# Kernel tuning notes

Measured on AMD Instinct MI355X. Metric: run time of the kernel, lower is better.

Reference implementation:

```python
import jax, jax.numpy as jnp
import numpy as np

SEQ = 2048
HID = 1024
NH = 16
HD = HID // NH


def setup_inputs() -> dict:
    key = jax.random.key(0)
    ks = jax.random.split(key, 5)
    s = 0.02
    return {
        "hidden_states": jax.random.normal(ks[0], (SEQ, HID), dtype=jnp.float32),
        "w_attn": jax.random.normal(ks[1], (HID, 3 * HID), dtype=jnp.float32) * s,
        "b_attn": jax.random.normal(ks[2], (3 * HID,), dtype=jnp.float32) * s,
        "w_proj": jax.random.normal(ks[3], (HID, HID), dtype=jnp.float32) * s,
        "b_proj": jax.random.normal(ks[4], (HID,), dtype=jnp.float32) * s,
    }


def reference(hidden_states, w_attn, b_attn, w_proj, b_proj):
    S = hidden_states.shape[0]
    qkv = hidden_states @ w_attn + b_attn          # [S, 3H]
    q, k, v = jnp.split(qkv, 3, axis=-1)
    q = q.reshape(S, NH, HD)
    k = k.reshape(S, NH, HD)
    v = v.reshape(S, NH, HD)
    sm_scale = 1.0 / np.sqrt(HD).astype(np.float32)
    # explicit scores [h, q, k] in fp32, as in the torch module
    scores = jnp.einsum('qhd,khd->hqk', q.astype(jnp.float32), k.astype(jnp.float32))
    scores = scores * sm_scale
    causal = jnp.tril(jnp.ones((S, S), dtype=bool))  # [q, k]
    scores = jnp.where(causal[None, :, :], scores, -jnp.inf)
    probs = jax.nn.softmax(scores, axis=-1)
    attn = jnp.einsum('hqk,khd->qhd', probs, v.astype(jnp.float32))  # [S, NH, HD]
    attn = attn.reshape(S, HID).astype(hidden_states.dtype)
    return attn @ w_proj + b_proj
```

## Files before the change

kernel.cpp:

```cpp
#include <hip/hip_runtime.h>
#include <cstdint>
#include <cstddef>

#define SEQ 2048
#define HID 1024
#define NHEAD 16
#define HDIM 64

typedef _Float16 f16;
typedef f16 half8 __attribute__((ext_vector_type(8)));
typedef f16 half4 __attribute__((ext_vector_type(4)));
typedef f16 half2_ __attribute__((ext_vector_type(2)));
typedef float f32x4 __attribute__((ext_vector_type(4)));

#define ASYNC_COPY16(g, l)                                                    \
  __builtin_amdgcn_global_load_lds(                                           \
      (const __attribute__((address_space(1))) void*)(const void*)(g),        \
      (__attribute__((address_space(3))) void*)(void*)(l), 16, 0, 0)

__global__ __launch_bounds__(256) void prologue(
    const float* __restrict__ h, const float* __restrict__ wa,
    const float* __restrict__ wp, f16* __restrict__ h16,
    f16* __restrict__ waT, f16* __restrict__ wpT) {
  const int b = blockIdx.x, tid = threadIdx.x;
  if (b >= 4096) {
    int i = ((b - 4096) * 256 + tid) * 4;
    float4 v = *(const float4*)(h + i);
    half4 o;
    o[0] = (f16)v.x; o[1] = (f16)v.y; o[2] = (f16)v.z; o[3] = (f16)v.w;
    *(half4*)(h16 + i) = o;
    return;
  }
  const float* src; f16* dst; int C, bx, by;
  if (b < 3072) { src = wa; dst = waT; C = 3072; bx = b % 96; by = b / 96; }
  else { int t = b - 3072; src = wp; dst = wpT; C = 1024; bx = t & 31; by = t >> 5; }
  __shared__ float tile[32][33];
  const int tx = tid & 31, ty = tid >> 5;
  const int c0 = bx * 32, r0 = by * 32;
#pragma unroll
  for (int i = 0; i < 32; i += 8)
    tile[ty + i][tx] = src[(size_t)(r0 + ty + i) * C + c0 + tx];
  __syncthreads();
#pragma unroll
  for (int i = 0; i < 32; i += 8)
    dst[(size_t)(c0 + ty + i) * 1024 + r0 + tx] = (f16)tile[tx][ty + i];
}

template <int BM, int BN, bool OUT16>
__global__ __launch_bounds__(256) void gemm_f16(
    const f16* __restrict__ A, const f16* __restrict__ Bt,
    const float* __restrict__ bias, void* __restrict__ Cout, int M, int N,
    int K) {
  constexpr int FM = BM / 32, FN = BN / 32;
  __shared__ __align__(16) f16 sA[BM * 64];
  __shared__ __align__(16) f16 sB[BN * 64];
  const int tid = threadIdx.x;
  const int wave = tid >> 6, lane = tid & 63;
  const int quad = lane >> 4, l16 = lane & 15;
  const int m0 = blockIdx.y * BM, n0 = blockIdx.x * BN;
  const int wm = (wave >> 1) * (BM / 2), wn = (wave & 1) * (BN / 2);
  const int rowA = lane >> 3;
  const int chunkA = (lane & 7) ^ rowA;
  const int r7 = l16 & 7;

  f32x4 acc[FM][FN] = {};

  for (int k0 = 0; k0 < K; k0 += 64) {
#pragma unroll
    for (int r = wave; r < BM / 8; r += 4)
      ASYNC_COPY16(A + (size_t)(m0 + r * 8 + rowA) * K + k0 + chunkA * 8,
                   &sA[r * 512]);
#pragma unroll
    for (int r = wave; r < BN / 8; r += 4)
      ASYNC_COPY16(Bt + (size_t)(n0 + r * 8 + rowA) * K + k0 + chunkA * 8,
                   &sB[r * 512]);
    __syncthreads();

#pragma unroll
    for (int h = 0; h < 2; h++) {
      half8 af[FM], bf[FN];
#pragma unroll
      for (int i = 0; i < FM; i++)
        af[i] = *(const half8*)&sA[(wm + i * 16 + l16) * 64 +
                                   (((h << 2) | quad) ^ r7) * 8];
#pragma unroll
      for (int j = 0; j < FN; j++)
        bf[j] = *(const half8*)&sB[(wn + j * 16 + l16) * 64 +
                                   (((h << 2) | quad) ^ r7) * 8];
#pragma unroll
      for (int i = 0; i < FM; i++)
#pragma unroll
        for (int j = 0; j < FN; j++)
          acc[i][j] = __builtin_amdgcn_mfma_f32_16x16x32_f16(
              af[i], bf[j], acc[i][j], 0, 0, 0);
    }
    __syncthreads();
  }

#pragma unroll
  for (int i = 0; i < FM; i++) {
    int row = m0 + wm + i * 16 + quad * 4;
#pragma unroll
    for (int j = 0; j < FN; j++) {
      int col = n0 + wn + j * 16 + l16;
      float bv = bias[col];
#pragma unroll
      for (int r = 0; r < 4; r++) {
        float v = acc[i][j][r] + bv;
        if (OUT16)
          ((f16*)Cout)[(size_t)(row + r) * N + col] = (f16)v;
        else
          ((float*)Cout)[(size_t)(row + r) * N + col] = v;
      }
    }
  }
}

#define LROW 72
__global__ __launch_bounds__(256, 3) void attn_split(
    const f16* __restrict__ qkv, f16* __restrict__ out,
    f16* __restrict__ Opart, float* __restrict__ ml) {
  const int b = (blockIdx.x & 7) * 80 + (blockIdx.x >> 3);
  const int h = b / 40;
  const int t = b % 40;
  int m, c, nc;
  if (t < 4)       { m = t;                 c = 0;      nc = 1; }
  else if (t < 12) { int u = t - 4;  m = 4 + (u >> 1);  c = u & 1; nc = 2; }
  else if (t < 24) { int u = t - 12; m = 8 + u / 3;     c = u % 3; nc = 3; }
  else             { int u = t - 24; m = 12 + (u >> 2); c = u & 3; nc = 4; }
  const int q0 = m * 128;
  const int T = 2 * m + 2;
  const int kt0 = c * 8;
  const int kt1 = (kt0 + 8 < T) ? kt0 + 8 : T;
  const int maskFrom = 2 * m;

  __shared__ __align__(16) f16 sK[64 * LROW];
  __shared__ __align__(16) f16 sVt[64 * LROW];
  __shared__ __align__(16) f16 sP[4][32 * LROW];

  const int tid = threadIdx.x;
  const int wave = tid >> 6, lane = tid & 63;
  const int quad = lane >> 4, l16 = lane & 15;

  const f16 qs = (f16)0.18033688f;
  half8 qf[2][2];
#pragma unroll
  for (int g = 0; g < 2; g++) {
    const f16* qb = qkv + (size_t)(q0 + wave * 32 + g * 16 + l16) * 3072 +
                    h * HDIM + quad * 8;
    qf[g][0] = *(const half8*)qb;
    qf[g][1] = *(const half8*)(qb + 32);
#pragma unroll
    for (int j = 0; j < 8; j++) { qf[g][0][j] *= qs; qf[g][1][j] *= qs; }
  }

  const f16* kbase = qkv + HID + h * HDIM;
  const f16* vbase = qkv + 2 * HID + h * HDIM;
  const int ks_row = tid >> 3, ks_cc = tid & 7;
  const int vs_d = tid & 63, vs_g = tid >> 6;

  f32x4 o[2][4] = {};
  float m_i[2] = {-1e30f, -1e30f}, l_i[2] = {0.f, 0.f};
  half8 kreg[2], vreg[2];

  auto prefetch = [&](int kt) {
    const int k0 = kt * 64;
#pragma unroll
    for (int i = 0; i < 2; i++) {
      kreg[i] = *(const half8*)(kbase + (size_t)(k0 + ks_row + i * 32) * 3072 +
                                ks_cc * 8);
      half8 col;
#pragma unroll
      for (int j = 0; j < 8; j++)
        col[j] = vbase[(size_t)(k0 + (vs_g + i * 4) * 8 + j) * 3072 + vs_d];
      vreg[i] = col;
    }
  };

  prefetch(kt0);
  for (int kt = kt0; kt < kt1; kt++) {
    const int k0 = kt * 64;
#pragma unroll
    for (int i = 0; i < 2; i++) {
      *(half8*)&sK[(ks_row + i * 32) * LROW + ks_cc * 8] = kreg[i];
      *(half8*)&sVt[vs_d * LROW + (vs_g + i * 4) * 8] = vreg[i];
    }
    __syncthreads();
    if (kt + 1 < kt1) prefetch(kt + 1);

    f32x4 sacc[2][4] = {};
#pragma unroll
    for (int kb = 0; kb < 4; kb++) {
      half8 kf0 = *(const half8*)&sK[(kb * 16 + l16) * LROW + quad * 8];
      half8 kf1 = *(const half8*)&sK[(kb * 16 + l16) * LROW + 32 + quad * 8];
#pragma unroll
      for (int g = 0; g < 2; g++) {
        sacc[g][kb] = __builtin_amdgcn_mfma_f32_16x16x32_f16(kf0, qf[g][0],
                                                             sacc[g][kb], 0, 0, 0);
        sacc[g][kb] = __builtin_amdgcn_mfma_f32_16x16x32_f16(kf1, qf[g][1],
                                                             sacc[g][kb], 0, 0, 0);
      }
    }
    if (kt >= maskFrom) {
#pragma unroll
      for (int g = 0; g < 2; g++) {
        const int qg = q0 + wave * 32 + g * 16 + l16;
#pragma unroll
        for (int kb = 0; kb < 4; kb++) {
          int kg = k0 + kb * 16 + quad * 4;
#pragma unroll
          for (int r = 0; r < 4; r++)
            if (kg + r > qg) sacc[g][kb][r] = -1e30f;
        }
      }
    }
#pragma unroll
    for (int g = 0; g < 2; g++) {
      float mx = -1e30f;
#pragma unroll
      for (int kb = 0; kb < 4; kb++)
#pragma unroll
        for (int r = 0; r < 4; r++) mx = fmaxf(mx, sacc[g][kb][r]);
      mx = fmaxf(mx, __shfl_xor(mx, 16));
      mx = fmaxf(mx, __shfl_xor(mx, 32));
      if (!__all(mx <= m_i[g] + 8.f)) {
        const float mnew = fmaxf(m_i[g], mx);
        const float alpha = exp2f(m_i[g] - mnew);
        l_i[g] *= alpha;
#pragma unroll
        for (int j = 0; j < 4; j++)
#pragma unroll
          for (int r = 0; r < 4; r++) o[g][j][r] *= alpha;
        m_i[g] = mnew;
      }
      float rs = 0.f;
#pragma unroll
      for (int kb = 0; kb < 4; kb++)
#pragma unroll
        for (int r = 0; r < 4; r++) {
          float p = exp2f(sacc[g][kb][r] - m_i[g]);
          sacc[g][kb][r] = p;
          rs += p;
        }
      rs += __shfl_xor(rs, 16);
      rs += __shfl_xor(rs, 32);
      l_i[g] += rs;
      f16* pw = &sP[wave][(g * 16 + l16) * LROW];
#pragma unroll
      for (int kb = 0; kb < 4; kb++)
#pragma unroll
        for (int rp = 0; rp < 2; rp++) {
          half2_ pv;
          pv[0] = (f16)sacc[g][kb][rp * 2];
          pv[1] = (f16)sacc[g][kb][rp * 2 + 1];
          *(half2_*)&pw[kb * 16 + quad * 4 + rp * 2] = pv;
        }
    }
    half8 pf[2][2];
#pragma unroll
    for (int g = 0; g < 2; g++) {
      pf[g][0] = *(const half8*)&sP[wave][(g * 16 + l16) * LROW + quad * 8];
      pf[g][1] = *(const half8*)&sP[wave][(g * 16 + l16) * LROW + 32 + quad * 8];
    }
#pragma unroll
    for (int j = 0; j < 4; j++) {
      half8 vf0 = *(const half8*)&sVt[(j * 16 + l16) * LROW + quad * 8];
      half8 vf1 = *(const half8*)&sVt[(j * 16 + l16) * LROW + 32 + quad * 8];
#pragma unroll
      for (int g = 0; g < 2; g++) {
        o[g][j] = __builtin_amdgcn_mfma_f32_16x16x32_f16(vf0, pf[g][0], o[g][j], 0, 0, 0);
        o[g][j] = __builtin_amdgcn_mfma_f32_16x16x32_f16(vf1, pf[g][1], o[g][j], 0, 0, 0);
      }
    }
    __syncthreads();
  }

  if (nc == 1) {
#pragma unroll
    for (int g = 0; g < 2; g++) {
      const float inv = 1.f / l_i[g];
      f16* orow =
          out + (size_t)(q0 + wave * 32 + g * 16 + l16) * HID + h * HDIM;
#pragma unroll
      for (int j = 0; j < 4; j++) {
        half4 hv;
#pragma unroll
        for (int r = 0; r < 4; r++) hv[r] = (f16)(o[g][j][r] * inv);
        *(half4*)&orow[j * 16 + quad * 4] = hv;
      }
    }
  } else {
    int base;
    if (m < 8)       base = (m - 4) * 2;
    else if (m < 12) base = 8 + (m - 8) * 3;
    else             base = 20 + (m - 12) * 4;
    const int slot = h * 36 + base + c;
#pragma unroll
    for (int g = 0; g < 2; g++) {
      const int qrow = wave * 32 + g * 16 + l16;
      f16* op = Opart + (size_t)slot * 8192 + qrow * 64;
#pragma unroll
      for (int j = 0; j < 4; j++) {
        half4 hv;
#pragma unroll
        for (int r = 0; r < 4; r++) hv[r] = (f16)o[g][j][r];
        *(half4*)&op[j * 16 + quad * 4] = hv;
      }
      if (quad == 0) {
        ml[slot * 256 + qrow] = m_i[g];
        ml[slot * 256 + 128 + qrow] = l_i[g];
      }
    }
  }
}

__global__ __launch_bounds__(256) void attn_combine(
    const f16* __restrict__ Opart, const float* __restrict__ ml,
    f16* __restrict__ out) {
  int idx = blockIdx.x * 256 + threadIdx.x;
  int d = idx & 63;
  int row = (idx >> 6) & 127;
  int rest = idx >> 13;
  int mi = rest % 12;
  int h = rest / 12;
  int m = 4 + mi;
  int nc = (mi < 4) ? 2 : (mi < 8) ? 3 : 4;
  int base = (mi < 4) ? mi * 2 : (mi < 8) ? 8 + (mi - 4) * 3 : 20 + (mi - 8) * 4;
  int slot0 = h * 36 + base;

  float mm[4], ll[4];
  float M = -1e30f;
  for (int cc = 0; cc < nc; cc++) {
    mm[cc] = ml[(slot0 + cc) * 256 + row];
    ll[cc] = ml[(slot0 + cc) * 256 + 128 + row];
    M = fmaxf(M, mm[cc]);
  }
  float L = 0.f, acc = 0.f;
  for (int cc = 0; cc < nc; cc++) {
    float w = exp2f(mm[cc] - M);
    L += w * ll[cc];
    acc += w * (float)Opart[(size_t)(slot0 + cc) * 8192 + row * 64 + d];
  }
  out[(size_t)(m * 128 + row) * HID + h * HDIM + d] = (f16)(acc / L);
}

extern "C" void kernel_launch(void* const* d_in, const int* in_sizes, int n_in,
                              void* d_out, int out_size, void* d_ws,
                              size_t ws_size, hipStream_t stream) {
  const float* h = (const float*)d_in[0];
  const float* wa = (const float*)d_in[1];
  const float* ba = (const float*)d_in[2];
  const float* wp = (const float*)d_in[3];
  const float* bp = (const float*)d_in[4];
  float* out = (float*)d_out;

  char* ws = (char*)d_ws;
  f16* h16 = (f16*)(ws);
  f16* waT = (f16*)(ws + (4u << 20));
  f16* wpT = (f16*)(ws + (10u << 20));
  f16* qkv = (f16*)(ws + (12u << 20));
  f16* attn = (f16*)(ws + (24u << 20));
  f16* Opart = (f16*)(ws);
  float* mlbuf = (float*)(ws + 9437184);

  prologue<<<6144, 256, 0, stream>>>(h, wa, wp, h16, waT, wpT);
  gemm_f16<64, 128, true><<<dim3(24, 32), 256, 0, stream>>>(
      h16, waT, ba, qkv, SEQ, 3 * HID, HID);
  attn_split<<<640, 256, 0, stream>>>(qkv, attn, Opart, mlbuf);
  attn_combine<<<6144, 256, 0, stream>>>(Opart, mlbuf, attn);
  gemm_f16<64, 64, false><<<dim3(16, 32), 256, 0, stream>>>(
      attn, wpT, bp, out, SEQ, HID, HID);
}
```

Before: 153.9 us.

## Fuse split-KV combine into attention via atomic last-block reduction; enlarge prologue tiles

Removes the separate attn_combine launch. Each split block now increments a per-(head, query-tile) counter after a threadfence, and the last-arriving block merges the partial O and m/l values into the final output with vectorized half4 loads. The prologue transpose tiles grow from 32x32 to 64x64 and the fp32-to-fp16 conversion processes 8 elements per thread. The prologue also zeroes the counters, which adds an atomic and a fence on every split block and puts combine work on the tail of the attention kernel.

```diff
diff --git a/kernel.cpp b/kernel.cpp
--- a/kernel.cpp
+++ b/kernel.cpp
@@ -21,28 +21,31 @@
 __global__ __launch_bounds__(256) void prologue(
     const float* __restrict__ h, const float* __restrict__ wa,
     const float* __restrict__ wp, f16* __restrict__ h16,
-    f16* __restrict__ waT, f16* __restrict__ wpT) {
+    f16* __restrict__ waT, f16* __restrict__ wpT, int* __restrict__ cnt) {
   const int b = blockIdx.x, tid = threadIdx.x;
-  if (b >= 4096) {
-    int i = ((b - 4096) * 256 + tid) * 4;
-    float4 v = *(const float4*)(h + i);
-    half4 o;
-    o[0] = (f16)v.x; o[1] = (f16)v.y; o[2] = (f16)v.z; o[3] = (f16)v.w;
-    *(half4*)(h16 + i) = o;
+  if (b >= 1024) {
+    if (b == 1024 && tid < 192) cnt[tid] = 0;
+    int i = ((b - 1024) * 256 + tid) * 8;
+    float4 v0 = *(const float4*)(h + i);
+    float4 v1 = *(const float4*)(h + i + 4);
+    half8 o;
+    o[0] = (f16)v0.x; o[1] = (f16)v0.y; o[2] = (f16)v0.z; o[3] = (f16)v0.w;
+    o[4] = (f16)v1.x; o[5] = (f16)v1.y; o[6] = (f16)v1.z; o[7] = (f16)v1.w;
+    *(half8*)(h16 + i) = o;
     return;
   }
   const float* src; f16* dst; int C, bx, by;
-  if (b < 3072) { src = wa; dst = waT; C = 3072; bx = b % 96; by = b / 96; }
-  else { int t = b - 3072; src = wp; dst = wpT; C = 1024; bx = t & 31; by = t >> 5; }
-  __shared__ float tile[32][33];
-  const int tx = tid & 31, ty = tid >> 5;
-  const int c0 = bx * 32, r0 = by * 32;
-#pragma unroll
-  for (int i = 0; i < 32; i += 8)
+  if (b < 768) { src = wa; dst = waT; C = 3072; bx = b % 48; by = b / 48; }
+  else { int t = b - 768; src = wp; dst = wpT; C = 1024; bx = t & 15; by = t >> 4; }
+  __shared__ float tile[64][65];
+  const int tx = tid & 63, ty = tid >> 6;
+  const int c0 = bx * 64, r0 = by * 64;
+#pragma unroll
+  for (int i = 0; i < 64; i += 4)
     tile[ty + i][tx] = src[(size_t)(r0 + ty + i) * C + c0 + tx];
   __syncthreads();
 #pragma unroll
-  for (int i = 0; i < 32; i += 8)
+  for (int i = 0; i < 64; i += 4)
     dst[(size_t)(c0 + ty + i) * 1024 + r0 + tx] = (f16)tile[tx][ty + i];
 }
 
@@ -119,7 +122,7 @@
 #define LROW 72
 __global__ __launch_bounds__(256, 3) void attn_split(
     const f16* __restrict__ qkv, f16* __restrict__ out,
-    f16* __restrict__ Opart, float* __restrict__ ml) {
+    f16* __restrict__ Opart, float* __restrict__ ml, int* __restrict__ cnt) {
   const int b = (blockIdx.x & 7) * 80 + (blockIdx.x >> 3);
   const int h = b / 40;
   const int t = b % 40;
@@ -137,6 +140,7 @@
   __shared__ __align__(16) f16 sK[64 * LROW];
   __shared__ __align__(16) f16 sVt[64 * LROW];
   __shared__ __align__(16) f16 sP[4][32 * LROW];
+  __shared__ int sLast;
 
   const int tid = threadIdx.x;
   const int wave = tid >> 6, lane = tid & 63;
@@ -311,37 +315,48 @@
         ml[slot * 256 + 128 + qrow] = l_i[g];
       }
     }
-  }
-}
-
-__global__ __launch_bounds__(256) void attn_combine(
-    const f16* __restrict__ Opart, const float* __restrict__ ml,
-    f16* __restrict__ out) {
-  int idx = blockIdx.x * 256 + threadIdx.x;
-  int d = idx & 63;
-  int row = (idx >> 6) & 127;
-  int rest = idx >> 13;
-  int mi = rest % 12;
-  int h = rest / 12;
-  int m = 4 + mi;
-  int nc = (mi < 4) ? 2 : (mi < 8) ? 3 : 4;
-  int base = (mi < 4) ? mi * 2 : (mi < 8) ? 8 + (mi - 4) * 3 : 20 + (mi - 8) * 4;
-  int slot0 = h * 36 + base;
-
-  float mm[4], ll[4];
-  float M = -1e30f;
-  for (int cc = 0; cc < nc; cc++) {
-    mm[cc] = ml[(slot0 + cc) * 256 + row];
-    ll[cc] = ml[(slot0 + cc) * 256 + 128 + row];
-    M = fmaxf(M, mm[cc]);
-  }
-  float L = 0.f, acc = 0.f;
-  for (int cc = 0; cc < nc; cc++) {
-    float w = exp2f(mm[cc] - M);
-    L += w * ll[cc];
-    acc += w * (float)Opart[(size_t)(slot0 + cc) * 8192 + row * 64 + d];
-  }
-  out[(size_t)(m * 128 + row) * HID + h * HDIM + d] = (f16)(acc / L);
+    __threadfence();
+    if (tid == 0) {
+      int prev = atomicAdd(&cnt[h * 12 + (m - 4)], 1);
+      sLast = (prev == nc - 1);
+    }
+    __syncthreads();
+    if (sLast) {
+      __threadfence();
+      const int slot0 = h * 36 + base;
+      const int row_l = tid >> 4;
+      const int d4 = (tid & 15) * 4;
+#pragma unroll
+      for (int pass = 0; pass < 8; pass++) {
+        const int row = pass * 16 + row_l;
+        float mm[4], ll[4];
+        float M = -1e30f;
+#pragma unroll
+        for (int cc = 0; cc < 4; cc++)
+          if (cc < nc) {
+            mm[cc] = ml[(slot0 + cc) * 256 + row];
+            ll[cc] = ml[(slot0 + cc) * 256 + 128 + row];
+            M = fmaxf(M, mm[cc]);
+          }
+        float L = 0.f, acc[4] = {0.f, 0.f, 0.f, 0.f};
+#pragma unroll
+        for (int cc = 0; cc < 4; cc++)
+          if (cc < nc) {
+            float w = exp2f(mm[cc] - M);
+            L += w * ll[cc];
+            half4 ov = *(const half4*)&Opart[(size_t)(slot0 + cc) * 8192 +
+                                             row * 64 + d4];
+#pragma unroll
+            for (int r = 0; r < 4; r++) acc[r] += w * (float)ov[r];
+          }
+        const float invL = 1.f / L;
+        half4 hv;
+#pragma unroll
+        for (int r = 0; r < 4; r++) hv[r] = (f16)(acc[r] * invL);
+        *(half4*)&out[(size_t)(q0 + row) * HID + h * HDIM + d4] = hv;
+      }
+    }
+  }
 }
 
 extern "C" void kernel_launch(void* const* d_in, const int* in_sizes, int n_in,
@@ -362,12 +377,12 @@
   f16* attn = (f16*)(ws + (24u << 20));
   f16* Opart = (f16*)(ws);
   float* mlbuf = (float*)(ws + 9437184);
-
-  prologue<<<6144, 256, 0, stream>>>(h, wa, wp, h16, waT, wpT);
+  int* cnt = (int*)(ws + (28u << 20));
+
+  prologue<<<2048, 256, 0, stream>>>(h, wa, wp, h16, waT, wpT, cnt);
   gemm_f16<64, 128, true><<<dim3(24, 32), 256, 0, stream>>>(
       h16, waT, ba, qkv, SEQ, 3 * HID, HID);
-  attn_split<<<640, 256, 0, stream>>>(qkv, attn, Opart, mlbuf);
-  attn_combine<<<6144, 256, 0, stream>>>(Opart, mlbuf, attn);
+  attn_split<<<640, 256, 0, stream>>>(qkv, attn, Opart, mlbuf, cnt);
   gemm_f16<64, 64, false><<<dim3(16, 32), 256, 0, stream>>>(
       attn, wpT, bp, out, SEQ, HID, HID);
 }
```

After: 248.9 us. 1.62x slower.
